# Kernel tuning notes

Hardware: AMD Instinct MI355X
Metric: run time of the kernel (lower is better)

## Reference

```python
import jax, jax.numpy as jnp
import numpy as np

B, T, C, H, L, V = 512, 128, 512, 8, 6, 13
D = C // H  # 64


def setup_inputs() -> dict:
    key = jax.random.key(0)
    ks = jax.random.split(key, 12)
    s = 0.02
    return {
        "token_idxs": jax.random.randint(ks[0], (B, T), 0, V),
        "label": jax.random.randint(ks[1], (B,), 0, V),
        "wte": jax.random.normal(ks[2], (V, C), jnp.float32) * s,
        "wpe": jax.random.normal(ks[3], (T, C), jnp.float32) * s,
        "Wq": jax.random.normal(ks[4], (L, C, C), jnp.float32) * s,
        "bq": jnp.zeros((L, C), jnp.float32),
        "Wk": jax.random.normal(ks[5], (L, C, C), jnp.float32) * s,
        "bk": jnp.zeros((L, C), jnp.float32),
        "Wv": jax.random.normal(ks[6], (L, C, C), jnp.float32) * s,
        "bv": jnp.zeros((L, C), jnp.float32),
        "Wo": jax.random.normal(ks[7], (L, C, C), jnp.float32) * s,
        "bo": jnp.zeros((L, C), jnp.float32),
        "ln_g": jnp.ones((L, C), jnp.float32),
        "ln_b": jnp.zeros((L, C), jnp.float32),
        "W_lm": jax.random.normal(ks[8], (C, V), jnp.float32) * s,
        "b_lm": jnp.zeros((V,), jnp.float32),
    }


def _layer_norm(x, g, b, eps=1e-5):
    m = jnp.mean(x, axis=-1, keepdims=True)
    v = jnp.var(x, axis=-1, keepdims=True)
    return (x - m) / jnp.sqrt(v + eps) * g + b


def reference(token_idxs, label, wte, wpe, Wq, bq, Wk, bk, Wv, bv, Wo, bo, ln_g, ln_b, W_lm, b_lm):
    b, t = token_idxs.shape
    x = wte[token_idxs] + wpe[jnp.arange(t)]  # [b,t,C]
    inv_sqrt_d = 1.0 / jnp.sqrt(jnp.float32(D))
    for i in range(L):
        q = (x @ Wq[i] + bq[i]).reshape(b, t, H, D)
        k = (x @ Wk[i] + bk[i]).reshape(b, t, H, D)
        v = (x @ Wv[i] + bv[i]).reshape(b, t, H, D)
        # NOTE: matches the source exactly: attention over the HEAD axis at
        # each (b,t) position -> att shape [b,t,H,H]
        att = jnp.einsum('bthd,btgd->bthg', q, k) * inv_sqrt_d
        att = jax.nn.softmax(att, axis=-1)
        hid = jnp.einsum('bthg,btgd->bthd', att, v).reshape(b, t, C)
        x = _layer_norm(hid @ Wo[i] + bo[i] + x, ln_g[i], ln_b[i])
    logits = x @ W_lm + b_lm  # [b,t,V]
    logp = jax.nn.log_softmax(logits[:, -1, :], axis=-1)
    loss = -jnp.take_along_axis(logp, label[:, None], axis=-1).mean()
    return logits, loss
```

## Files before the change

kernel.cpp:

```cpp
#include <hip/hip_runtime.h>
#include <hip/hip_bf16.h>
#include <cstdint>
#include <cstddef>


typedef __attribute__((ext_vector_type(8))) short short8;
typedef __attribute__((ext_vector_type(4))) float f32x4;

__device__ __forceinline__ float bf2f(ushort u) {
    return __uint_as_float(((unsigned int)u) << 16);
}
__device__ __forceinline__ ushort f2bf(float f) {
    unsigned int x = __float_as_uint(f);
    unsigned int r = (x + 0x7fffu + ((x >> 16) & 1u)) >> 16;
    return (ushort)r;
}
__device__ __forceinline__ void gload_lds16(const void* g, void* l) {
    __builtin_amdgcn_global_load_lds(
        (const __attribute__((address_space(1))) void*)g,
        (__attribute__((address_space(3))) void*)l, 16, 0, 0);
}

__global__ __launch_bounds__(256) void prep_all(
    const float* __restrict__ Wq, const float* __restrict__ Wk,
    const float* __restrict__ Wv, const float* __restrict__ Wo,
    const float* __restrict__ wte, const float* __restrict__ wpe,
    const float* __restrict__ ln_g, const float* __restrict__ ln_b,
    ushort* __restrict__ wqkvT, ushort* __restrict__ woT,
    ushort* __restrict__ tmp0, float* __restrict__ s_qkv,
    float* __restrict__ t_qkv, float* __restrict__ psA,
    float* __restrict__ pssA, float* __restrict__ ones,
    float* __restrict__ zeros) {
    __shared__ float lds[64][65];
    __shared__ float gld[64], bld[64];
    __shared__ float sred[4][64], tred[4][64];
    const int bid = blockIdx.x;
    const int tid = threadIdx.x;
    if (bid < 192) {
        const int mat = bid >> 3;
        const int tc = bid & 7;
        const int l = mat >> 2, which = mat & 3;
        const float* S;
        switch (which) {
            case 0: S = Wq; break;
            case 1: S = Wk; break;
            case 2: S = Wv; break;
            default: S = Wo; break;
        }
        S += (size_t)l * 262144;
        ushort* T = (which < 3) ? wqkvT + (size_t)l * 786432 + which * 262144
                                : woT + (size_t)l * 262144;
        const bool fold = (which < 3);
        const float* g = (fold && l > 0) ? ln_g + (l - 1) * 512 : nullptr;
        const float* b = (fold && l > 0) ? ln_b + (l - 1) * 512 : nullptr;
        const int c = tid & 63;
        float sp = 0.f, tp = 0.f;
        for (int tr = 0; tr < 8; tr++) {
            __syncthreads();
            #pragma unroll
            for (int it = 0; it < 16; it++) {
                int r = it * 4 + (tid >> 6);
                lds[r][c] = S[(size_t)(tr * 64 + r) * 512 + tc * 64 + c];
            }
            if (tid < 64) {
                gld[tid] = g ? g[tr * 64 + tid] : 1.f;
                bld[tid] = b ? b[tr * 64 + tid] : 0.f;
            }
            __syncthreads();
            float gk = fold ? gld[c] : 1.f;
            #pragma unroll
            for (int it = 0; it < 16; it++) {
                int rn = it * 4 + (tid >> 6);
                float val = lds[c][rn] * gk;
                T[(size_t)(tc * 64 + rn) * 512 + tr * 64 + c] = f2bf(val);
            }
            if (fold) {
                #pragma unroll
                for (int i = 0; i < 16; i++) {
                    int kl = (tid >> 6) * 16 + i;
                    float w = lds[kl][c];
                    sp += gld[kl] * w;
                    tp += bld[kl] * w;
                }
            }
        }
        if (fold) {
            __syncthreads();
            sred[tid >> 6][c] = sp;
            tred[tid >> 6][c] = tp;
            __syncthreads();
            if (tid < 64) {
                float ss = sred[0][tid] + sred[1][tid] + sred[2][tid] + sred[3][tid];
                float tt = tred[0][tid] + tred[1][tid] + tred[2][tid] + tred[3][tid];
                int o = l * 1536 + which * 512 + tc * 64 + tid;
                s_qkv[o] = ss;
                t_qkv[o] = tt;
            }
        }
    } else if (bid < 608) {
        size_t idx = (size_t)(bid - 192) * 256 + tid;
        size_t u = idx >> 6;
        int c8 = (int)(idx & 63);
        int v = (int)(u >> 7);
        int t = (int)(u & 127);
        const float* ep = wte + (size_t)v * 512 + c8 * 8;
        const float* pp = wpe + (size_t)t * 512 + c8 * 8;
        float4 e0 = *(const float4*)ep, e1 = *(const float4*)(ep + 4);
        float4 p0 = *(const float4*)pp, p1 = *(const float4*)(pp + 4);
        float s[8] = {e0.x + p0.x, e0.y + p0.y, e0.z + p0.z, e0.w + p0.w,
                      e1.x + p1.x, e1.y + p1.y, e1.z + p1.z, e1.w + p1.w};
        short8 o;
        #pragma unroll
        for (int j = 0; j < 8; j++) o[j] = (short)f2bf(s[j]);
        *(short8*)(tmp0 + u * 512 + c8 * 8) = o;
    } else if (bid < 660) {
        int i = (bid - 608) * 256 + tid;
        if (i < 6656) psA[i] = 0.f;
        else {
            int j = i - 6656;
            pssA[j] = (j < 1664) ? 511.99488f : 0.f;
        }
    } else {
        ones[tid] = 1.f;  ones[tid + 256] = 1.f;
        zeros[tid] = 0.f; zeros[tid + 256] = 0.f;
    }
}

__global__ __launch_bounds__(256) void qkv_fold(
    const ushort* __restrict__ A, const float* __restrict__ psin,
    const float* __restrict__ pssin, const ushort* __restrict__ Bt,
    const float* __restrict__ s_l, const float* __restrict__ t_l,
    const float* __restrict__ b0, const float* __restrict__ b1,
    const float* __restrict__ b2, ushort* __restrict__ obf) {
    __shared__ alignas(16) ushort As[2][64 * 64];
    __shared__ alignas(16) ushort Bs[2][128 * 64];
    __shared__ float smu[64], srs[64];
    const int tid = threadIdx.x;
    const int lane = tid & 63;
    const int wave = tid >> 6;
    const int m0 = blockIdx.x * 64;
    const int n0 = blockIdx.y * 128;
    const int wm = (wave >> 1) * 32;
    const int wn = (wave & 1) * 64;
    const int r = lane & 15;
    const int kq = (lane >> 4) * 8;
    const ushort* Ab = A  + (size_t)m0 * 512;
    const ushort* Bb = Bt + (size_t)n0 * 512;
    f32x4 acc[2][4] = {};

    auto stage = [&](int t, int b) {
        const ushort* At = Ab + t * 64;
        const ushort* Bt2 = Bb + t * 64;
        #pragma unroll
        for (int i = 0; i < 2; i++) {
            int cb = (i * 4 + wave) * 64;
            int ch = cb + lane;
            int row = ch >> 3;
            int c8 = (ch & 7) ^ (row & 7);
            gload_lds16(At + (size_t)row * 512 + c8 * 8, (char*)As[b] + cb * 16);
        }
        #pragma unroll
        for (int i = 0; i < 4; i++) {
            int cb = (i * 4 + wave) * 64;
            int ch = cb + lane;
            int row = ch >> 3;
            int c8 = (ch & 7) ^ (row & 7);
            gload_lds16(Bt2 + (size_t)row * 512 + c8 * 8, (char*)Bs[b] + cb * 16);
        }
    };

    stage(0, 0);
    if (tid < 64) {
        int row = m0 + tid;
        float s  = psin[row] + psin[1664 + row] + psin[3328 + row] + psin[4992 + row];
        float ss = pssin[row] + pssin[1664 + row] + pssin[3328 + row] + pssin[4992 + row];
        float mean = s * (1.f / 512.f);
        float var = ss * (1.f / 512.f) - mean * mean;
        smu[tid] = mean;
        srs[tid] = rsqrtf(var + 1e-5f);
    }
    __syncthreads();
    #pragma unroll
    for (int t = 0; t < 8; t++) {
        const int cur = t & 1;
        if (t < 7) stage(t + 1, cur ^ 1);
        #pragma unroll
        for (int kk = 0; kk < 64; kk += 32) {
            short8 af[2], bfr[4];
            #pragma unroll
            for (int m = 0; m < 2; m++) {
                int row = wm + m * 16 + r;
                int boff = (row * 128 + (kk + kq) * 2) ^ ((row & 7) << 4);
                af[m] = *(const short8*)((const char*)As[cur] + boff);
            }
            #pragma unroll
            for (int n = 0; n < 4; n++) {
                int row = wn + n * 16 + r;
                int boff = (row * 128 + (kk + kq) * 2) ^ ((row & 7) << 4);
                bfr[n] = *(const short8*)((const char*)Bs[cur] + boff);
            }
            #pragma unroll
            for (int m = 0; m < 2; m++)
                #pragma unroll
                for (int n = 0; n < 4; n++)
                    acc[m][n] = __builtin_amdgcn_mfma_f32_16x16x32_bf16(
                        af[m], bfr[n], acc[m][n], 0, 0, 0);
        }
        __syncthreads();
    }
    const int r4 = (lane >> 4) * 4;
    const int cc = lane & 15;
    #pragma unroll
    for (int m = 0; m < 2; m++) {
        #pragma unroll
        for (int n = 0; n < 4; n++) {
            int cg = n0 + wn + n * 16 + cc;
            float bias = (cg < 512) ? b0[cg] : (cg < 1024) ? b1[cg - 512] : b2[cg - 1024];
            float sc = s_l[cg];
            float tc_ = t_l[cg] + bias;
            #pragma unroll
            for (int i = 0; i < 4; i++) {
                int lrow = wm + m * 16 + r4 + i;
                float v = srs[lrow] * (acc[m][n][i] - smu[lrow] * sc) + tc_;
                obf[(size_t)(m0 + lrow) * 1536 + cg] = f2bf(v);
            }
        }
    }
}

__global__ __launch_bounds__(256) void attn_kernel(const ushort* __restrict__ qkv,
                                                   ushort* __restrict__ hid) {
    const int lane = threadIdx.x & 63;
    const size_t pos = (size_t)blockIdx.x * 4 + (threadIdx.x >> 6);
    const ushort* base = qkv + pos * 1536;
    const int h = lane >> 3, g = lane & 7;
    const ushort* qp = base + h * 64;
    const ushort* kp = base + 512 + g * 64;
    float s = 0.f;
    #pragma unroll
    for (int dc = 0; dc < 8; dc++) {
        short8 q8 = *(const short8*)(qp + dc * 8);
        short8 k8 = *(const short8*)(kp + dc * 8);
        #pragma unroll
        for (int j = 0; j < 8; j++) s += bf2f((ushort)q8[j]) * bf2f((ushort)k8[j]);
    }
    s *= 0.125f;
    float mx = s;
    #pragma unroll
    for (int o = 1; o < 8; o <<= 1) mx = fmaxf(mx, __shfl_xor(mx, o));
    float e = __expf(s - mx);
    float den = e;
    #pragma unroll
    for (int o = 1; o < 8; o <<= 1) den += __shfl_xor(den, o);
    float att = e / den;
    float o8[8];
    #pragma unroll
    for (int j = 0; j < 8; j++) o8[j] = 0.f;
    const ushort* vp = base + 1024 + (lane & 7) * 8;
    #pragma unroll
    for (int gg = 0; gg < 8; gg++) {
        float a = __shfl(att, (lane & 56) | gg);
        short8 v8 = *(const short8*)(vp + gg * 64);
        #pragma unroll
        for (int j = 0; j < 8; j++) o8[j] += a * bf2f((ushort)v8[j]);
    }
    short8 ov;
    #pragma unroll
    for (int j = 0; j < 8; j++) ov[j] = (short)f2bf(o8[j]);
    *(short8*)(hid + pos * 512 + lane * 8) = ov;
}

__global__ __launch_bounds__(256) void proj_fold(
    const ushort* __restrict__ A, const ushort* __restrict__ Bt,
    const float* __restrict__ bo_, const float* __restrict__ psin,
    const float* __restrict__ pssin, const float* __restrict__ g_in,
    const float* __restrict__ b_in, ushort* tmp,
    float* __restrict__ psout, float* __restrict__ pssout) {
    __shared__ alignas(16) ushort As[2][32 * 64];
    __shared__ alignas(16) ushort Bs[2][128 * 64];
    __shared__ float lps[2][32], lpss[2][32];
    __shared__ float smu[32], srs[32];
    const int tid = threadIdx.x;
    const int lane = tid & 63;
    const int wave = tid >> 6;
    const int m0 = blockIdx.x * 32;
    const int n0 = blockIdx.y * 128;
    const int wm = (wave >> 1) * 16;
    const int wn = (wave & 1) * 64;
    const int r = lane & 15;
    const int kq = (lane >> 4) * 8;
    const ushort* Ab = A  + (size_t)m0 * 512;
    const ushort* Bb = Bt + (size_t)n0 * 512;
    f32x4 acc[4] = {};

    auto stage = [&](int t, int b) {
        const ushort* At = Ab + t * 64;
        const ushort* Bt2 = Bb + t * 64;
        {
            int cb = wave * 64;
            int ch = cb + lane;
            int row = ch >> 3;
            int c8 = (ch & 7) ^ (row & 7);
            gload_lds16(At + (size_t)row * 512 + c8 * 8, (char*)As[b] + cb * 16);
        }
        #pragma unroll
        for (int i = 0; i < 4; i++) {
            int cb = (i * 4 + wave) * 64;
            int ch = cb + lane;
            int row = ch >> 3;
            int c8 = (ch & 7) ^ (row & 7);
            gload_lds16(Bt2 + (size_t)row * 512 + c8 * 8, (char*)Bs[b] + cb * 16);
        }
    };

    stage(0, 0);
    if (tid < 32) {
        int row = m0 + tid;
        float s  = psin[row] + psin[1664 + row] + psin[3328 + row] + psin[4992 + row];
        float ss = pssin[row] + pssin[1664 + row] + pssin[3328 + row] + pssin[4992 + row];
        float mean = s * (1.f / 512.f);
        float var = ss * (1.f / 512.f) - mean * mean;
        smu[tid] = mean;
        srs[tid] = rsqrtf(var + 1e-5f);
    }
    __syncthreads();
    #pragma unroll
    for (int t = 0; t < 8; t++) {
        const int cur = t & 1;
        if (t < 7) stage(t + 1, cur ^ 1);
        #pragma unroll
        for (int kk = 0; kk < 64; kk += 32) {
            int arow = wm + r;
            int aoff = (arow * 128 + (kk + kq) * 2) ^ ((arow & 7) << 4);
            short8 af = *(const short8*)((const char*)As[cur] + aoff);
            #pragma unroll
            for (int n = 0; n < 4; n++) {
                int brow = wn + n * 16 + r;
                int boff = (brow * 128 + (kk + kq) * 2) ^ ((brow & 7) << 4);
                short8 bfr = *(const short8*)((const char*)Bs[cur] + boff);
                acc[n] = __builtin_amdgcn_mfma_f32_16x16x32_bf16(
                    af, bfr, acc[n], 0, 0, 0);
            }
        }
        __syncthreads();
    }

    const int r4 = (lane >> 4) * 4;
    const int cc = lane & 15;
    float s_i[4] = {0.f, 0.f, 0.f, 0.f}, ss_i[4] = {0.f, 0.f, 0.f, 0.f};
    #pragma unroll
    for (int n = 0; n < 4; n++) {
        int col = n0 + wn + n * 16 + cc;
        float boc = bo_[col];
        float gc = g_in[col], bc = b_in[col];
        #pragma unroll
        for (int i = 0; i < 4; i++) {
            int lr = wm + r4 + i;
            int rg = m0 + lr;
            float resid = (bf2f(tmp[(size_t)rg * 512 + col]) - smu[lr])
                          * srs[lr] * gc + bc;
            float v = acc[n][i] + boc + resid;
            tmp[(size_t)rg * 512 + col] = f2bf(v);
            s_i[i] += v; ss_i[i] += v * v;
        }
    }
    #pragma unroll
    for (int i = 0; i < 4; i++) {
        #pragma unroll
        for (int o = 1; o < 16; o <<= 1) {
            s_i[i] += __shfl_xor(s_i[i], o);
            ss_i[i] += __shfl_xor(ss_i[i], o);
        }
    }
    if (cc == 0) {
        #pragma unroll
        for (int i = 0; i < 4; i++) {
            lps[wn >> 6][wm + r4 + i] = s_i[i];
            lpss[wn >> 6][wm + r4 + i] = ss_i[i];
        }
    }
    __syncthreads();
    if (tid < 32) {
        int row = m0 + tid;
        psout[blockIdx.y * 1664 + row]  = lps[0][tid] + lps[1][tid];
        pssout[blockIdx.y * 1664 + row] = lpss[0][tid] + lpss[1][tid];
    }
}

__global__ __launch_bounds__(256) void logits_ln(
    const ushort* __restrict__ tin, const float* __restrict__ psin,
    const float* __restrict__ pssin, const float* __restrict__ gv,
    const float* __restrict__ bv, const float* __restrict__ Wlm,
    const float* __restrict__ blm, float* __restrict__ lu) {
    __shared__ float wl[8 * 64 * 13];
    const int tid = threadIdx.x;
    for (int k = tid; k < 512; k += 256) {
        int dst = ((k & 7) * 64 + (k >> 3)) * 13;
        #pragma unroll
        for (int v = 0; v < 13; v++) wl[dst + v] = Wlm[k * 13 + v];
    }
    __syncthreads();
    const int lane = tid & 63;
    const int w = tid >> 6;
    const int c0 = lane * 8;
    float4 g0 = *(const float4*)(gv + c0), g1 = *(const float4*)(gv + c0 + 4);
    float4 b0 = *(const float4*)(bv + c0), b1 = *(const float4*)(bv + c0 + 4);
    float gg[8] = {g0.x, g0.y, g0.z, g0.w, g1.x, g1.y, g1.z, g1.w};
    float bb[8] = {b0.x, b0.y, b0.z, b0.w, b1.x, b1.y, b1.z, b1.w};
    float bl[13];
    #pragma unroll
    for (int v = 0; v < 13; v++) bl[v] = blm[v];
    for (int it = 0; it < 8; it++) {
        size_t row = (size_t)blockIdx.x * 32 + it * 4 + w;
        float s  = psin[row] + psin[1664 + row] + psin[3328 + row] + psin[4992 + row];
        float ss = pssin[row] + pssin[1664 + row] + pssin[3328 + row] + pssin[4992 + row];
        float mean = s * (1.f / 512.f);
        float rstd = rsqrtf(ss * (1.f / 512.f) - mean * mean + 1e-5f);
        short8 xv = *(const short8*)(tin + row * 512 + c0);
        float p[13];
        #pragma unroll
        for (int v = 0; v < 13; v++) p[v] = 0.f;
        #pragma unroll
        for (int j = 0; j < 8; j++) {
            float xf = (bf2f((ushort)xv[j]) - mean) * rstd * gg[j] + bb[j];
            const float* wr = wl + (j * 64 + lane) * 13;
            #pragma unroll
            for (int v = 0; v < 13; v++) p[v] += xf * wr[v];
        }
        #pragma unroll
        for (int v = 0; v < 13; v++) {
            #pragma unroll
            for (int o = 32; o > 0; o >>= 1) p[v] += __shfl_xor(p[v], o);
        }
        if (lane == 0) {
            #pragma unroll
            for (int v = 0; v < 13; v++) lu[row * 13 + v] = p[v] + bl[v];
        }
    }
}

__global__ __launch_bounds__(256) void scatter_loss(
    const float* __restrict__ lu, const int* __restrict__ tok,
    const int* __restrict__ label, float* __restrict__ out) {
    __shared__ float red[4];
    const int tid = threadIdx.x;
    if (blockIdx.x < 3328) {
        unsigned int i = blockIdx.x * 256 + tid;
        unsigned int bt = i / 13u;
        unsigned int vv = i - bt * 13u;
        int v = tok[bt];
        int t = (int)(bt & 127u);
        out[i] = lu[(size_t)((v << 7) + t) * 13 + vv];
    } else {
        float acc = 0.f;
        for (int b = tid; b < 512; b += 256) {
            int v = tok[b * 128 + 127];
            const float* lg = lu + (size_t)((v << 7) + 127) * 13;
            float mx = lg[0];
            #pragma unroll
            for (int vv = 1; vv < 13; vv++) mx = fmaxf(mx, lg[vv]);
            float den = 0.f;
            #pragma unroll
            for (int vv = 0; vv < 13; vv++) den += expf(lg[vv] - mx);
            int lab = label[b];
            acc += -(lg[lab] - mx - logf(den));
        }
        #pragma unroll
        for (int o = 32; o > 0; o >>= 1) acc += __shfl_xor(acc, o);
        if ((tid & 63) == 0) red[tid >> 6] = acc;
        __syncthreads();
        if (tid == 0)
            out[851968] = (red[0] + red[1] + red[2] + red[3]) * (1.f / 512.f);
    }
}

extern "C" void kernel_launch(void* const* d_in, const int* in_sizes, int n_in,
                              void* d_out, int out_size, void* d_ws, size_t ws_size,
                              hipStream_t stream) {
    const int*   tok   = (const int*)d_in[0];
    const int*   label = (const int*)d_in[1];
    const float* wte   = (const float*)d_in[2];
    const float* wpe   = (const float*)d_in[3];
    const float* Wq    = (const float*)d_in[4];
    const float* bq    = (const float*)d_in[5];
    const float* Wk    = (const float*)d_in[6];
    const float* bk    = (const float*)d_in[7];
    const float* Wv    = (const float*)d_in[8];
    const float* bv    = (const float*)d_in[9];
    const float* Wo    = (const float*)d_in[10];
    const float* bo    = (const float*)d_in[11];
    const float* ln_g  = (const float*)d_in[12];
    const float* ln_b  = (const float*)d_in[13];
    const float* Wlm   = (const float*)d_in[14];
    const float* blm   = (const float*)d_in[15];
    float* out = (float*)d_out;

    char* ws = (char*)d_ws;
    ushort* wqkvT = (ushort*)(ws);
    ushort* woT   = (ushort*)(ws + 9437184);
    ushort* qkv_u = (ushort*)(ws + 12582912);
    ushort* hid_u = (ushort*)(ws + 17694720);
    ushort* tmp   = (ushort*)(ws + 19398656);
    float*  psA   = (float*) (ws + 21102592);
    float*  pssA  = (float*) (ws + 21129216);
    float*  psB   = (float*) (ws + 21155840);
    float*  pssB  = (float*) (ws + 21182464);
    float*  lu    = (float*) (ws + 21209088);
    float*  s_qkv = (float*) (ws + 21295616);
    float*  t_qkv = (float*) (ws + 21332480);
    float*  ones  = (float*) (ws + 21369344);
    float*  zeros = (float*) (ws + 21371392);

    prep_all<<<661, 256, 0, stream>>>(Wq, Wk, Wv, Wo, wte, wpe, ln_g, ln_b,
                                      wqkvT, woT, tmp, s_qkv, t_qkv,
                                      psA, pssA, ones, zeros);

    const float *psin = psA, *pssin = pssA;
    float *psout = psB, *pssout = pssB;
    for (int l = 0; l < 6; l++) {
        const float* g_in = (l == 0) ? ones  : ln_g + (l - 1) * 512;
        const float* b_in = (l == 0) ? zeros : ln_b + (l - 1) * 512;
        qkv_fold<<<dim3(26, 12), 256, 0, stream>>>(
            tmp, psin, pssin, wqkvT + (size_t)l * 786432,
            s_qkv + l * 1536, t_qkv + l * 1536,
            bq + l * 512, bk + l * 512, bv + l * 512, qkv_u);
        attn_kernel<<<416, 256, 0, stream>>>(qkv_u, hid_u);
        proj_fold<<<dim3(52, 4), 256, 0, stream>>>(
            hid_u, woT + (size_t)l * 262144, bo + l * 512,
            psin, pssin, g_in, b_in, tmp, psout, pssout);
        const float* p1 = psin;  psin = psout;  psout = (float*)p1;
        const float* p2 = pssin; pssin = pssout; pssout = (float*)p2;
    }

    logits_ln<<<52, 256, 0, stream>>>(tmp, psin, pssin,
                                      ln_g + 5 * 512, ln_b + 5 * 512, Wlm, blm, lu);
    scatter_loss<<<3329, 256, 0, stream>>>(lu, tok, label, out);
}
```

Measured before the change: 220.4 us.

## Fuse all transformer layers into one persistent kernel with grid barriers

Replaces the 19 per-layer launches (qkv GEMM, head attention, output projection, logits) with a single persistent kernel of 416 blocks. Phases are separated by a software grid barrier built from hierarchical atomic counters, and the barrier memory is cleared with a memset beforehand. This removes launch overhead and inter-kernel gaps for small GEMMs, but relies on all 416 blocks being co-resident (launch bounds set to 2 blocks per CU) and leaves many blocks idle during the GEMM phases.

New measurement: 612.4 us. +177.9%, slower.

```diff
diff --git a/kernel.cpp b/kernel.cpp
--- a/kernel.cpp
+++ b/kernel.cpp
@@ -7,6 +7,8 @@
 typedef __attribute__((ext_vector_type(8))) short short8;
 typedef __attribute__((ext_vector_type(4))) float f32x4;
 
+#define NBLK 416
+
 __device__ __forceinline__ float bf2f(ushort u) {
     return __uint_as_float(((unsigned int)u) << 16);
 }
@@ -19,6 +21,24 @@
     __builtin_amdgcn_global_load_lds(
         (const __attribute__((address_space(1))) void*)g,
         (__attribute__((address_space(3))) void*)l, 16, 0, 0);
+}
+
+__device__ __forceinline__ void gridbar(unsigned int* bar, int idx) {
+    __syncthreads();
+    if (threadIdx.x == 0) {
+        __threadfence();
+        unsigned int* cell = bar + (size_t)(idx * 9 + (blockIdx.x & 7)) * 16;
+        unsigned int* done = bar + (size_t)(idx * 9 + 8) * 16;
+        unsigned int old = atomicAdd(cell, 1u);
+        if (old == 51u) atomicAdd(done, 1u);
+        unsigned int tries = 0;
+        while (__hip_atomic_load(done, __ATOMIC_RELAXED,
+                                 __HIP_MEMORY_SCOPE_AGENT) < 8u &&
+               ++tries < 50000000u)
+            __builtin_amdgcn_s_sleep(2);
+        __threadfence();
+    }
+    __syncthreads();
 }
 
 __global__ __launch_bounds__(256) void prep_all(
@@ -126,315 +146,330 @@
     }
 }
 
-__global__ __launch_bounds__(256) void qkv_fold(
-    const ushort* __restrict__ A, const float* __restrict__ psin,
-    const float* __restrict__ pssin, const ushort* __restrict__ Bt,
-    const float* __restrict__ s_l, const float* __restrict__ t_l,
-    const float* __restrict__ b0, const float* __restrict__ b1,
-    const float* __restrict__ b2, ushort* __restrict__ obf) {
-    __shared__ alignas(16) ushort As[2][64 * 64];
-    __shared__ alignas(16) ushort Bs[2][128 * 64];
+__global__ __launch_bounds__(256, 2) void net_kernel(
+    const ushort* __restrict__ wqkvT, const ushort* __restrict__ woT,
+    ushort* __restrict__ qkv_u, ushort* __restrict__ hid_u,
+    ushort* __restrict__ tmp,
+    float* __restrict__ psA, float* __restrict__ pssA,
+    float* __restrict__ psB, float* __restrict__ pssB,
+    const float* __restrict__ s_qkv, const float* __restrict__ t_qkv,
+    const float* __restrict__ bq, const float* __restrict__ bk,
+    const float* __restrict__ bv, const float* __restrict__ bo,
+    const float* __restrict__ ln_g, const float* __restrict__ ln_b,
+    const float* __restrict__ ones, const float* __restrict__ zeros,
+    const float* __restrict__ Wlm, const float* __restrict__ blm,
+    float* __restrict__ lu, unsigned int* __restrict__ bar) {
+    __shared__ alignas(16) char smem[49152];
     __shared__ float smu[64], srs[64];
+    __shared__ float lps[2][32], lpss[2][32];
+    const int bid = blockIdx.x;
     const int tid = threadIdx.x;
     const int lane = tid & 63;
     const int wave = tid >> 6;
-    const int m0 = blockIdx.x * 64;
-    const int n0 = blockIdx.y * 128;
-    const int wm = (wave >> 1) * 32;
-    const int wn = (wave & 1) * 64;
     const int r = lane & 15;
     const int kq = (lane >> 4) * 8;
-    const ushort* Ab = A  + (size_t)m0 * 512;
-    const ushort* Bb = Bt + (size_t)n0 * 512;
-    f32x4 acc[2][4] = {};
-
-    auto stage = [&](int t, int b) {
-        const ushort* At = Ab + t * 64;
-        const ushort* Bt2 = Bb + t * 64;
-        #pragma unroll
-        for (int i = 0; i < 2; i++) {
-            int cb = (i * 4 + wave) * 64;
-            int ch = cb + lane;
-            int row = ch >> 3;
-            int c8 = (ch & 7) ^ (row & 7);
-            gload_lds16(At + (size_t)row * 512 + c8 * 8, (char*)As[b] + cb * 16);
-        }
-        #pragma unroll
-        for (int i = 0; i < 4; i++) {
-            int cb = (i * 4 + wave) * 64;
-            int ch = cb + lane;
-            int row = ch >> 3;
-            int c8 = (ch & 7) ^ (row & 7);
-            gload_lds16(Bt2 + (size_t)row * 512 + c8 * 8, (char*)Bs[b] + cb * 16);
-        }
-    };
-
-    stage(0, 0);
-    if (tid < 64) {
-        int row = m0 + tid;
-        float s  = psin[row] + psin[1664 + row] + psin[3328 + row] + psin[4992 + row];
-        float ss = pssin[row] + pssin[1664 + row] + pssin[3328 + row] + pssin[4992 + row];
-        float mean = s * (1.f / 512.f);
-        float var = ss * (1.f / 512.f) - mean * mean;
-        smu[tid] = mean;
-        srs[tid] = rsqrtf(var + 1e-5f);
-    }
-    __syncthreads();
-    #pragma unroll
-    for (int t = 0; t < 8; t++) {
-        const int cur = t & 1;
-        if (t < 7) stage(t + 1, cur ^ 1);
-        #pragma unroll
-        for (int kk = 0; kk < 64; kk += 32) {
-            short8 af[2], bfr[4];
-            #pragma unroll
-            for (int m = 0; m < 2; m++) {
-                int row = wm + m * 16 + r;
-                int boff = (row * 128 + (kk + kq) * 2) ^ ((row & 7) << 4);
-                af[m] = *(const short8*)((const char*)As[cur] + boff);
-            }
-            #pragma unroll
-            for (int n = 0; n < 4; n++) {
-                int row = wn + n * 16 + r;
-                int boff = (row * 128 + (kk + kq) * 2) ^ ((row & 7) << 4);
-                bfr[n] = *(const short8*)((const char*)Bs[cur] + boff);
-            }
-            #pragma unroll
-            for (int m = 0; m < 2; m++)
-                #pragma unroll
-                for (int n = 0; n < 4; n++)
-                    acc[m][n] = __builtin_amdgcn_mfma_f32_16x16x32_bf16(
-                        af[m], bfr[n], acc[m][n], 0, 0, 0);
-        }
-        __syncthreads();
-    }
     const int r4 = (lane >> 4) * 4;
     const int cc = lane & 15;
-    #pragma unroll
-    for (int m = 0; m < 2; m++) {
+
+    const float* psin = psA;  const float* pssin = pssA;
+    float* psout = psB;       float* pssout = pssB;
+
+    for (int l = 0; l < 6; l++) {
+        if (bid < 312) {
+            ushort (*As)[64 * 64] = (ushort (*)[64 * 64])smem;
+            ushort (*Bs)[128 * 64] = (ushort (*)[128 * 64])(smem + 16384);
+            const int m0 = (bid % 26) * 64;
+            const int n0 = (bid / 26) * 128;
+            const int wm = (wave >> 1) * 32;
+            const int wn = (wave & 1) * 64;
+            const ushort* Ab = tmp + (size_t)m0 * 512;
+            const ushort* Bb = wqkvT + (size_t)l * 786432 + (size_t)n0 * 512;
+            f32x4 acc[2][4] = {};
+
+            auto stage = [&](int t, int b) {
+                const ushort* At = Ab + t * 64;
+                const ushort* Bt2 = Bb + t * 64;
+                #pragma unroll
+                for (int i = 0; i < 2; i++) {
+                    int cb = (i * 4 + wave) * 64;
+                    int ch = cb + lane;
+                    int row = ch >> 3;
+                    int c8 = (ch & 7) ^ (row & 7);
+                    gload_lds16(At + (size_t)row * 512 + c8 * 8,
+                                (char*)As[b] + cb * 16);
+                }
+                #pragma unroll
+                for (int i = 0; i < 4; i++) {
+                    int cb = (i * 4 + wave) * 64;
+                    int ch = cb + lane;
+                    int row = ch >> 3;
+                    int c8 = (ch & 7) ^ (row & 7);
+                    gload_lds16(Bt2 + (size_t)row * 512 + c8 * 8,
+                                (char*)Bs[b] + cb * 16);
+                }
+            };
+
+            stage(0, 0);
+            if (tid < 64) {
+                int row = m0 + tid;
+                float s  = psin[row] + psin[1664 + row] + psin[3328 + row] + psin[4992 + row];
+                float ss = pssin[row] + pssin[1664 + row] + pssin[3328 + row] + pssin[4992 + row];
+                float mean = s * (1.f / 512.f);
+                float var = ss * (1.f / 512.f) - mean * mean;
+                smu[tid] = mean;
+                srs[tid] = rsqrtf(var + 1e-5f);
+            }
+            __syncthreads();
+            #pragma unroll
+            for (int t = 0; t < 8; t++) {
+                const int cur = t & 1;
+                if (t < 7) stage(t + 1, cur ^ 1);
+                #pragma unroll
+                for (int kk = 0; kk < 64; kk += 32) {
+                    short8 af[2], bfr[4];
+                    #pragma unroll
+                    for (int m = 0; m < 2; m++) {
+                        int row = wm + m * 16 + r;
+                        int boff = (row * 128 + (kk + kq) * 2) ^ ((row & 7) << 4);
+                        af[m] = *(const short8*)((const char*)As[cur] + boff);
+                    }
+                    #pragma unroll
+                    for (int n = 0; n < 4; n++) {
+                        int row = wn + n * 16 + r;
+                        int boff = (row * 128 + (kk + kq) * 2) ^ ((row & 7) << 4);
+                        bfr[n] = *(const short8*)((const char*)Bs[cur] + boff);
+                    }
+                    #pragma unroll
+                    for (int m = 0; m < 2; m++)
+                        #pragma unroll
+                        for (int n = 0; n < 4; n++)
+                            acc[m][n] = __builtin_amdgcn_mfma_f32_16x16x32_bf16(
+                                af[m], bfr[n], acc[m][n], 0, 0, 0);
+                }
+                __syncthreads();
+            }
+            const float* s_l = s_qkv + l * 1536;
+            const float* t_l = t_qkv + l * 1536;
+            #pragma unroll
+            for (int m = 0; m < 2; m++) {
+                #pragma unroll
+                for (int n = 0; n < 4; n++) {
+                    int cg = n0 + wn + n * 16 + cc;
+                    float bias = (cg < 512) ? bq[l * 512 + cg]
+                               : (cg < 1024) ? bk[l * 512 + cg - 512]
+                                             : bv[l * 512 + cg - 1024];
+                    float sc = s_l[cg];
+                    float tc_ = t_l[cg] + bias;
+                    #pragma unroll
+                    for (int i = 0; i < 4; i++) {
+                        int lrow = wm + m * 16 + r4 + i;
+                        float v = srs[lrow] * (acc[m][n][i] - smu[lrow] * sc) + tc_;
+                        qkv_u[(size_t)(m0 + lrow) * 1536 + cg] = f2bf(v);
+                    }
+                }
+            }
+        }
+        gridbar(bar, l * 3 + 0);
+
+        {
+            const size_t pos = (size_t)bid * 4 + wave;
+            const ushort* base = qkv_u + pos * 1536;
+            const int h = lane >> 3, g = lane & 7;
+            const ushort* qp = base + h * 64;
+            const ushort* kp = base + 512 + g * 64;
+            float s = 0.f;
+            #pragma unroll
+            for (int dc = 0; dc < 8; dc++) {
+                short8 q8 = *(const short8*)(qp + dc * 8);
+                short8 k8 = *(const short8*)(kp + dc * 8);
+                #pragma unroll
+                for (int j = 0; j < 8; j++) s += bf2f((ushort)q8[j]) * bf2f((ushort)k8[j]);
+            }
+            s *= 0.125f;
+            float mx = s;
+            #pragma unroll
+            for (int o = 1; o < 8; o <<= 1) mx = fmaxf(mx, __shfl_xor(mx, o));
+            float e = __expf(s - mx);
+            float den = e;
+            #pragma unroll
+            for (int o = 1; o < 8; o <<= 1) den += __shfl_xor(den, o);
+            float att = e / den;
+            float o8[8];
+            #pragma unroll
+            for (int j = 0; j < 8; j++) o8[j] = 0.f;
+            const ushort* vp = base + 1024 + (lane & 7) * 8;
+            #pragma unroll
+            for (int gg = 0; gg < 8; gg++) {
+                float a = __shfl(att, (lane & 56) | gg);
+                short8 v8 = *(const short8*)(vp + gg * 64);
+                #pragma unroll
+                for (int j = 0; j < 8; j++) o8[j] += a * bf2f((ushort)v8[j]);
+            }
+            short8 ov;
+            #pragma unroll
+            for (int j = 0; j < 8; j++) ov[j] = (short)f2bf(o8[j]);
+            *(short8*)(hid_u + pos * 512 + lane * 8) = ov;
+        }
+        gridbar(bar, l * 3 + 1);
+
+        if (bid < 208) {
+            ushort (*As)[32 * 64] = (ushort (*)[32 * 64])smem;
+            ushort (*Bs)[128 * 64] = (ushort (*)[128 * 64])(smem + 16384);
+            const int m0 = (bid % 52) * 32;
+            const int nb = bid / 52;
+            const int n0 = nb * 128;
+            const int wm = (wave >> 1) * 16;
+            const int wn = (wave & 1) * 64;
+            const ushort* Ab = hid_u + (size_t)m0 * 512;
+            const ushort* Bb = woT + (size_t)l * 262144 + (size_t)n0 * 512;
+            const float* g_in = (l == 0) ? ones  : ln_g + (l - 1) * 512;
+            const float* b_in = (l == 0) ? zeros : ln_b + (l - 1) * 512;
+            f32x4 acc[4] = {};
+
+            auto stage = [&](int t, int b) {
+                const ushort* At = Ab + t * 64;
+                const ushort* Bt2 = Bb + t * 64;
+                {
+                    int cb = wave * 64;
+                    int ch = cb + lane;
+                    int row = ch >> 3;
+                    int c8 = (ch & 7) ^ (row & 7);
+                    gload_lds16(At + (size_t)row * 512 + c8 * 8,
+                                (char*)As[b] + cb * 16);
+                }
+                #pragma unroll
+                for (int i = 0; i < 4; i++) {
+                    int cb = (i * 4 + wave) * 64;
+                    int ch = cb + lane;
+                    int row = ch >> 3;
+                    int c8 = (ch & 7) ^ (row & 7);
+                    gload_lds16(Bt2 + (size_t)row * 512 + c8 * 8,
+                                (char*)Bs[b] + cb * 16);
+                }
+            };
+
+            stage(0, 0);
+            if (tid < 32) {
+                int row = m0 + tid;
+                float s  = psin[row] + psin[1664 + row] + psin[3328 + row] + psin[4992 + row];
+                float ss = pssin[row] + pssin[1664 + row] + pssin[3328 + row] + pssin[4992 + row];
+                float mean = s * (1.f / 512.f);
+                float var = ss * (1.f / 512.f) - mean * mean;
+                smu[tid] = mean;
+                srs[tid] = rsqrtf(var + 1e-5f);
+            }
+            __syncthreads();
+            #pragma unroll
+            for (int t = 0; t < 8; t++) {
+                const int cur = t & 1;
+                if (t < 7) stage(t + 1, cur ^ 1);
+                #pragma unroll
+                for (int kk = 0; kk < 64; kk += 32) {
+                    int arow = wm + r;
+                    int aoff = (arow * 128 + (kk + kq) * 2) ^ ((arow & 7) << 4);
+                    short8 af = *(const short8*)((const char*)As[cur] + aoff);
+                    #pragma unroll
+                    for (int n = 0; n < 4; n++) {
+                        int brow = wn + n * 16 + r;
+                        int boff = (brow * 128 + (kk + kq) * 2) ^ ((brow & 7) << 4);
+                        short8 bfr = *(const short8*)((const char*)Bs[cur] + boff);
+                        acc[n] = __builtin_amdgcn_mfma_f32_16x16x32_bf16(
+                            af, bfr, acc[n], 0, 0, 0);
+                    }
+                }
+                __syncthreads();
+            }
+            float s_i[4] = {0.f, 0.f, 0.f, 0.f}, ss_i[4] = {0.f, 0.f, 0.f, 0.f};
+            #pragma unroll
+            for (int n = 0; n < 4; n++) {
+                int col = n0 + wn + n * 16 + cc;
+                float boc = bo[l * 512 + col];
+                float gc = g_in[col], bc = b_in[col];
+                #pragma unroll
+                for (int i = 0; i < 4; i++) {
+                    int lr = wm + r4 + i;
+                    int rg = m0 + lr;
+                    float resid = (bf2f(tmp[(size_t)rg * 512 + col]) - smu[lr])
+                                  * srs[lr] * gc + bc;
+                    float v = acc[n][i] + boc + resid;
+                    tmp[(size_t)rg * 512 + col] = f2bf(v);
+                    s_i[i] += v; ss_i[i] += v * v;
+                }
+            }
+            #pragma unroll
+            for (int i = 0; i < 4; i++) {
+                #pragma unroll
+                for (int o = 1; o < 16; o <<= 1) {
+                    s_i[i] += __shfl_xor(s_i[i], o);
+                    ss_i[i] += __shfl_xor(ss_i[i], o);
+                }
+            }
+            if (cc == 0) {
+                #pragma unroll
+                for (int i = 0; i < 4; i++) {
+                    lps[wn >> 6][wm + r4 + i] = s_i[i];
+                    lpss[wn >> 6][wm + r4 + i] = ss_i[i];
+                }
+            }
+            __syncthreads();
+            if (tid < 32) {
+                int row = m0 + tid;
+                psout[nb * 1664 + row]  = lps[0][tid] + lps[1][tid];
+                pssout[nb * 1664 + row] = lpss[0][tid] + lpss[1][tid];
+            }
+        }
+        gridbar(bar, l * 3 + 2);
+
+        {
+            const float* p1 = psin;  psin = psout;  psout = (float*)p1;
+            const float* p2 = pssin; pssin = pssout; pssout = (float*)p2;
+        }
+    }
+
+    if (bid < 52) {
+        float* wl = (float*)smem;
+        for (int k = tid; k < 512; k += 256) {
+            int dst = ((k & 7) * 64 + (k >> 3)) * 13;
+            #pragma unroll
+            for (int v = 0; v < 13; v++) wl[dst + v] = Wlm[k * 13 + v];
+        }
+        __syncthreads();
+        const float* gv = ln_g + 5 * 512;
+        const float* bv2 = ln_b + 5 * 512;
+        const int c0 = lane * 8;
+        float4 g0 = *(const float4*)(gv + c0), g1 = *(const float4*)(gv + c0 + 4);
+        float4 b0 = *(const float4*)(bv2 + c0), b1 = *(const float4*)(bv2 + c0 + 4);
+        float gg[8] = {g0.x, g0.y, g0.z, g0.w, g1.x, g1.y, g1.z, g1.w};
+        float bb[8] = {b0.x, b0.y, b0.z, b0.w, b1.x, b1.y, b1.z, b1.w};
+        float bl[13];
         #pragma unroll
-        for (int n = 0; n < 4; n++) {
-            int cg = n0 + wn + n * 16 + cc;
-            float bias = (cg < 512) ? b0[cg] : (cg < 1024) ? b1[cg - 512] : b2[cg - 1024];
-            float sc = s_l[cg];
-            float tc_ = t_l[cg] + bias;
-            #pragma unroll
-            for (int i = 0; i < 4; i++) {
-                int lrow = wm + m * 16 + r4 + i;
-                float v = srs[lrow] * (acc[m][n][i] - smu[lrow] * sc) + tc_;
-                obf[(size_t)(m0 + lrow) * 1536 + cg] = f2bf(v);
-            }
-        }
-    }
-}
-
-__global__ __launch_bounds__(256) void attn_kernel(const ushort* __restrict__ qkv,
-                                                   ushort* __restrict__ hid) {
-    const int lane = threadIdx.x & 63;
-    const size_t pos = (size_t)blockIdx.x * 4 + (threadIdx.x >> 6);
-    const ushort* base = qkv + pos * 1536;
-    const int h = lane >> 3, g = lane & 7;
-    const ushort* qp = base + h * 64;
-    const ushort* kp = base + 512 + g * 64;
-    float s = 0.f;
-    #pragma unroll
-    for (int dc = 0; dc < 8; dc++) {
-        short8 q8 = *(const short8*)(qp + dc * 8);
-        short8 k8 = *(const short8*)(kp + dc * 8);
-        #pragma unroll
-        for (int j = 0; j < 8; j++) s += bf2f((ushort)q8[j]) * bf2f((ushort)k8[j]);
-    }
-    s *= 0.125f;
-    float mx = s;
-    #pragma unroll
-    for (int o = 1; o < 8; o <<= 1) mx = fmaxf(mx, __shfl_xor(mx, o));
-    float e = __expf(s - mx);
-    float den = e;
-    #pragma unroll
-    for (int o = 1; o < 8; o <<= 1) den += __shfl_xor(den, o);
-    float att = e / den;
-    float o8[8];
-    #pragma unroll
-    for (int j = 0; j < 8; j++) o8[j] = 0.f;
-    const ushort* vp = base + 1024 + (lane & 7) * 8;
-    #pragma unroll
-    for (int gg = 0; gg < 8; gg++) {
-        float a = __shfl(att, (lane & 56) | gg);
-        short8 v8 = *(const short8*)(vp + gg * 64);
-        #pragma unroll
-        for (int j = 0; j < 8; j++) o8[j] += a * bf2f((ushort)v8[j]);
-    }
-    short8 ov;
-    #pragma unroll
-    for (int j = 0; j < 8; j++) ov[j] = (short)f2bf(o8[j]);
-    *(short8*)(hid + pos * 512 + lane * 8) = ov;
-}
-
-__global__ __launch_bounds__(256) void proj_fold(
-    const ushort* __restrict__ A, const ushort* __restrict__ Bt,
-    const float* __restrict__ bo_, const float* __restrict__ psin,
-    const float* __restrict__ pssin, const float* __restrict__ g_in,
-    const float* __restrict__ b_in, ushort* tmp,
-    float* __restrict__ psout, float* __restrict__ pssout) {
-    __shared__ alignas(16) ushort As[2][32 * 64];
-    __shared__ alignas(16) ushort Bs[2][128 * 64];
-    __shared__ float lps[2][32], lpss[2][32];
-    __shared__ float smu[32], srs[32];
-    const int tid = threadIdx.x;
-    const int lane = tid & 63;
-    const int wave = tid >> 6;
-    const int m0 = blockIdx.x * 32;
-    const int n0 = blockIdx.y * 128;
-    const int wm = (wave >> 1) * 16;
-    const int wn = (wave & 1) * 64;
-    const int r = lane & 15;
-    const int kq = (lane >> 4) * 8;
-    const ushort* Ab = A  + (size_t)m0 * 512;
-    const ushort* Bb = Bt + (size_t)n0 * 512;
-    f32x4 acc[4] = {};
-
-    auto stage = [&](int t, int b) {
-        const ushort* At = Ab + t * 64;
-        const ushort* Bt2 = Bb + t * 64;
-        {
-            int cb = wave * 64;
-            int ch = cb + lane;
-            int row = ch >> 3;
-            int c8 = (ch & 7) ^ (row & 7);
-            gload_lds16(At + (size_t)row * 512 + c8 * 8, (char*)As[b] + cb * 16);
-        }
-        #pragma unroll
-        for (int i = 0; i < 4; i++) {
-            int cb = (i * 4 + wave) * 64;
-            int ch = cb + lane;
-            int row = ch >> 3;
-            int c8 = (ch & 7) ^ (row & 7);
-            gload_lds16(Bt2 + (size_t)row * 512 + c8 * 8, (char*)Bs[b] + cb * 16);
-        }
-    };
-
-    stage(0, 0);
-    if (tid < 32) {
-        int row = m0 + tid;
-        float s  = psin[row] + psin[1664 + row] + psin[3328 + row] + psin[4992 + row];
-        float ss = pssin[row] + pssin[1664 + row] + pssin[3328 + row] + pssin[4992 + row];
-        float mean = s * (1.f / 512.f);
-        float var = ss * (1.f / 512.f) - mean * mean;
-        smu[tid] = mean;
-        srs[tid] = rsqrtf(var + 1e-5f);
-    }
-    __syncthreads();
-    #pragma unroll
-    for (int t = 0; t < 8; t++) {
-        const int cur = t & 1;
-        if (t < 7) stage(t + 1, cur ^ 1);
-        #pragma unroll
-        for (int kk = 0; kk < 64; kk += 32) {
-            int arow = wm + r;
-            int aoff = (arow * 128 + (kk + kq) * 2) ^ ((arow & 7) << 4);
-            short8 af = *(const short8*)((const char*)As[cur] + aoff);
-            #pragma unroll
-            for (int n = 0; n < 4; n++) {
-                int brow = wn + n * 16 + r;
-                int boff = (brow * 128 + (kk + kq) * 2) ^ ((brow & 7) << 4);
-                short8 bfr = *(const short8*)((const char*)Bs[cur] + boff);
-                acc[n] = __builtin_amdgcn_mfma_f32_16x16x32_bf16(
-                    af, bfr, acc[n], 0, 0, 0);
-            }
-        }
-        __syncthreads();
-    }
-
-    const int r4 = (lane >> 4) * 4;
-    const int cc = lane & 15;
-    float s_i[4] = {0.f, 0.f, 0.f, 0.f}, ss_i[4] = {0.f, 0.f, 0.f, 0.f};
-    #pragma unroll
-    for (int n = 0; n < 4; n++) {
-        int col = n0 + wn + n * 16 + cc;
-        float boc = bo_[col];
-        float gc = g_in[col], bc = b_in[col];
-        #pragma unroll
-        for (int i = 0; i < 4; i++) {
-            int lr = wm + r4 + i;
-            int rg = m0 + lr;
-            float resid = (bf2f(tmp[(size_t)rg * 512 + col]) - smu[lr])
-                          * srs[lr] * gc + bc;
-            float v = acc[n][i] + boc + resid;
-            tmp[(size_t)rg * 512 + col] = f2bf(v);
-            s_i[i] += v; ss_i[i] += v * v;
-        }
-    }
-    #pragma unroll
-    for (int i = 0; i < 4; i++) {
-        #pragma unroll
-        for (int o = 1; o < 16; o <<= 1) {
-            s_i[i] += __shfl_xor(s_i[i], o);
-            ss_i[i] += __shfl_xor(ss_i[i], o);
-        }
-    }
-    if (cc == 0) {
-        #pragma unroll
-        for (int i = 0; i < 4; i++) {
-            lps[wn >> 6][wm + r4 + i] = s_i[i];
-            lpss[wn >> 6][wm + r4 + i] = ss_i[i];
-        }
-    }
-    __syncthreads();
-    if (tid < 32) {
-        int row = m0 + tid;
-        psout[blockIdx.y * 1664 + row]  = lps[0][tid] + lps[1][tid];
-        pssout[blockIdx.y * 1664 + row] = lpss[0][tid] + lpss[1][tid];
-    }
-}
-
-__global__ __launch_bounds__(256) void logits_ln(
-    const ushort* __restrict__ tin, const float* __restrict__ psin,
-    const float* __restrict__ pssin, const float* __restrict__ gv,
-    const float* __restrict__ bv, const float* __restrict__ Wlm,
-    const float* __restrict__ blm, float* __restrict__ lu) {
-    __shared__ float wl[8 * 64 * 13];
-    const int tid = threadIdx.x;
-    for (int k = tid; k < 512; k += 256) {
-        int dst = ((k & 7) * 64 + (k >> 3)) * 13;
-        #pragma unroll
-        for (int v = 0; v < 13; v++) wl[dst + v] = Wlm[k * 13 + v];
-    }
-    __syncthreads();
-    const int lane = tid & 63;
-    const int w = tid >> 6;
-    const int c0 = lane * 8;
-    float4 g0 = *(const float4*)(gv + c0), g1 = *(const float4*)(gv + c0 + 4);
-    float4 b0 = *(const float4*)(bv + c0), b1 = *(const float4*)(bv + c0 + 4);
-    float gg[8] = {g0.x, g0.y, g0.z, g0.w, g1.x, g1.y, g1.z, g1.w};
-    float bb[8] = {b0.x, b0.y, b0.z, b0.w, b1.x, b1.y, b1.z, b1.w};
-    float bl[13];
-    #pragma unroll
-    for (int v = 0; v < 13; v++) bl[v] = blm[v];
-    for (int it = 0; it < 8; it++) {
-        size_t row = (size_t)blockIdx.x * 32 + it * 4 + w;
-        float s  = psin[row] + psin[1664 + row] + psin[3328 + row] + psin[4992 + row];
-        float ss = pssin[row] + pssin[1664 + row] + pssin[3328 + row] + pssin[4992 + row];
-        float mean = s * (1.f / 512.f);
-        float rstd = rsqrtf(ss * (1.f / 512.f) - mean * mean + 1e-5f);
-        short8 xv = *(const short8*)(tin + row * 512 + c0);
-        float p[13];
-        #pragma unroll
-        for (int v = 0; v < 13; v++) p[v] = 0.f;
-        #pragma unroll
-        for (int j = 0; j < 8; j++) {
-            float xf = (bf2f((ushort)xv[j]) - mean) * rstd * gg[j] + bb[j];
-            const float* wr = wl + (j * 64 + lane) * 13;
-            #pragma unroll
-            for (int v = 0; v < 13; v++) p[v] += xf * wr[v];
-        }
-        #pragma unroll
-        for (int v = 0; v < 13; v++) {
-            #pragma unroll
-            for (int o = 32; o > 0; o >>= 1) p[v] += __shfl_xor(p[v], o);
-        }
-        if (lane == 0) {
-            #pragma unroll
-            for (int v = 0; v < 13; v++) lu[row * 13 + v] = p[v] + bl[v];
+        for (int v = 0; v < 13; v++) bl[v] = blm[v];
+        for (int it = 0; it < 8; it++) {
+            size_t row = (size_t)bid * 32 + it * 4 + wave;
+            float s  = psin[row] + psin[1664 + row] + psin[3328 + row] + psin[4992 + row];
+            float ss = pssin[row] + pssin[1664 + row] + pssin[3328 + row] + pssin[4992 + row];
+            float mean = s * (1.f / 512.f);
+            float rstd = rsqrtf(ss * (1.f / 512.f) - mean * mean + 1e-5f);
+            short8 xv = *(const short8*)(tmp + row * 512 + c0);
+            float p[13];
+            #pragma unroll
+            for (int v = 0; v < 13; v++) p[v] = 0.f;
+            #pragma unroll
+            for (int j = 0; j < 8; j++) {
+                float xf = (bf2f((ushort)xv[j]) - mean) * rstd * gg[j] + bb[j];
+                const float* wr = wl + (j * 64 + lane) * 13;
+                #pragma unroll
+                for (int v = 0; v < 13; v++) p[v] += xf * wr[v];
+            }
+            #pragma unroll
+            for (int v = 0; v < 13; v++) {
+                #pragma unroll
+                for (int o = 32; o > 0; o >>= 1) p[v] += __shfl_xor(p[v], o);
+            }
+            if (lane == 0) {
+                #pragma unroll
+                for (int v = 0; v < 13; v++) lu[row * 13 + v] = p[v] + bl[v];
+            }
         }
     }
 }
@@ -510,29 +545,15 @@
     float*  t_qkv = (float*) (ws + 21332480);
     float*  ones  = (float*) (ws + 21369344);
     float*  zeros = (float*) (ws + 21371392);
-
+    unsigned int* bar = (unsigned int*)(ws + 21373440);
+
+    hipMemsetAsync(bar, 0, 10368, stream);
     prep_all<<<661, 256, 0, stream>>>(Wq, Wk, Wv, Wo, wte, wpe, ln_g, ln_b,
                                       wqkvT, woT, tmp, s_qkv, t_qkv,
                                       psA, pssA, ones, zeros);
-
-    const float *psin = psA, *pssin = pssA;
-    float *psout = psB, *pssout = pssB;
-    for (int l = 0; l < 6; l++) {
-        const float* g_in = (l == 0) ? ones  : ln_g + (l - 1) * 512;
-        const float* b_in = (l == 0) ? zeros : ln_b + (l - 1) * 512;
-        qkv_fold<<<dim3(26, 12), 256, 0, stream>>>(
-            tmp, psin, pssin, wqkvT + (size_t)l * 786432,
-            s_qkv + l * 1536, t_qkv + l * 1536,
-            bq + l * 512, bk + l * 512, bv + l * 512, qkv_u);
-        attn_kernel<<<416, 256, 0, stream>>>(qkv_u, hid_u);
-        proj_fold<<<dim3(52, 4), 256, 0, stream>>>(
-            hid_u, woT + (size_t)l * 262144, bo + l * 512,
-            psin, pssin, g_in, b_in, tmp, psout, pssout);
-        const float* p1 = psin;  psin = psout;  psout = (float*)p1;
-        const float* p2 = pssin; pssin = pssout; pssout = (float*)p2;
-    }
-
-    logits_ln<<<52, 256, 0, stream>>>(tmp, psin, pssin,
-                                      ln_g + 5 * 512, ln_b + 5 * 512, Wlm, blm, lu);
+    net_kernel<<<NBLK, 256, 0, stream>>>(
+        wqkvT, woT, qkv_u, hid_u, tmp, psA, pssA, psB, pssB,
+        s_qkv, t_qkv, bq, bk, bv, bo, ln_g, ln_b, ones, zeros,
+        Wlm, blm, lu, bar);
     scatter_loss<<<3329, 256, 0, stream>>>(lu, tok, label, out);
 }
```
